# Performance work log

Measured on AMD Instinct MI355X. Metric: run time of the kernel, lower is better.

## Reference

```python
import jax, jax.numpy as jnp
import numpy as np
from jax import lax

B, T, C = 8, 1025, 512
HEADS = 8
CACHE = 256          # int(dim * cache_ratio)
CLS = 1
L = 256              # gr_cache memory length
H = W = 32           # sqrt(T - CLS)
EPS = 1e-5


def setup_inputs() -> dict:
    key = jax.random.key(0)
    ks = jax.random.split(key, 40)
    def w(k, shape, scale=0.02):
        return jax.random.normal(k, shape, dtype=jnp.float32) * scale
    inp = {}
    inp['x'] = jax.random.normal(ks[0], (B, T, C), dtype=jnp.float32)
    inp['gr_cache'] = jax.random.normal(ks[1], (1, L, CACHE), dtype=jnp.float32)
    # self-attention (dim=512) params, weights stored (in, out)
    inp['Wq1'] = w(ks[2], (C, C)); inp['bq1'] = jnp.zeros((C,), jnp.float32)
    inp['Wk1'] = w(ks[3], (C, C)); inp['bk1'] = jnp.zeros((C,), jnp.float32)
    inp['Wv1'] = w(ks[4], (C, C)); inp['bv1'] = jnp.zeros((C,), jnp.float32)
    inp['Wo1'] = w(ks[5], (C, C)); inp['bo1'] = jnp.zeros((C,), jnp.float32)
    # memory attention (dim=cache_dim=256) params
    inp['Wq2'] = w(ks[6], (CACHE, CACHE)); inp['bq2'] = jnp.zeros((CACHE,), jnp.float32)
    inp['Wk2'] = w(ks[7], (CACHE, CACHE)); inp['bk2'] = jnp.zeros((CACHE,), jnp.float32)
    inp['Wv2'] = w(ks[8], (CACHE, CACHE)); inp['bv2'] = jnp.zeros((CACHE,), jnp.float32)
    inp['Wo2'] = w(ks[9], (CACHE, CACHE)); inp['bo2'] = jnp.zeros((CACHE,), jnp.float32)
    # GRU-style gate linears: in = 2*cache_dim, out = cache_dim
    inp['Wr'] = w(ks[10], (2 * CACHE, CACHE)); inp['br'] = jnp.zeros((CACHE,), jnp.float32)
    inp['Wz'] = w(ks[11], (2 * CACHE, CACHE)); inp['bz'] = jnp.zeros((CACHE,), jnp.float32)
    inp['Wa'] = w(ks[12], (2 * CACHE, CACHE)); inp['ba'] = jnp.zeros((CACHE,), jnp.float32)
    # LayerNorm(cache_dim)
    inp['gamma'] = jnp.ones((CACHE,), jnp.float32)
    inp['beta'] = jnp.zeros((CACHE,), jnp.float32)
    # per-head gate logits, init to -1 as in the module
    inp['lam'] = jnp.full((HEADS,), -1.0, dtype=jnp.float32)
    # grouped conv pos-emb: Conv2d(512, 512, k=3, groups=CACHE) -> (O=512, I/g=2, 3, 3)
    inp['conv_w'] = w(ks[13], (C, C // CACHE, 3, 3))
    inp['conv_b'] = jnp.zeros((C,), jnp.float32)
    return inp


def _mha(q_in, kv_in, Wq, bq, Wk, bk, Wv, bv, Wo, bo):
    Bq, Tq, D = q_in.shape
    Tk = kv_in.shape[1]
    dh = D // HEADS
    q = (q_in @ Wq + bq).reshape(Bq, Tq, HEADS, dh)
    k = (kv_in @ Wk + bk).reshape(Bq, Tk, HEADS, dh)
    v = (kv_in @ Wv + bv).reshape(Bq, Tk, HEADS, dh)
    s = jnp.einsum('bqhd,bkhd->bhqk', q, k) * (1.0 / np.sqrt(dh)).astype(np.float32)
    a = jax.nn.softmax(s, axis=-1)
    o = jnp.einsum('bhqk,bkhd->bqhd', a, v).reshape(Bq, Tq, D)
    return o @ Wo + bo


def reference(x, gr_cache, Wq1, bq1, Wk1, bk1, Wv1, bv1, Wo1, bo1,
              Wq2, bq2, Wk2, bk2, Wv2, bv2, Wo2, bo2,
              Wr, br, Wz, bz, Wa, ba, gamma, beta, lam, conv_w, conv_b):
    B_, T_, C_ = x.shape
    # ---- spatial positional embedding (faithful to torch view->permute quirk) ----
    tok = x[:, CLS:, :].reshape(B_, H, W, C_).transpose(0, 3, 1, 2)   # (B, C, H, W)
    pos = lax.conv_general_dilated(tok, conv_w, (1, 1), 'SAME',
                                   feature_group_count=CACHE,
                                   dimension_numbers=('NCHW', 'OIHW', 'NCHW'))
    pos = pos + conv_b[None, :, None, None]
    pos = pos.reshape(B_, C_, T_ - CLS).transpose(0, 2, 1)            # (B, T-1, C)
    pos = jnp.concatenate([jnp.zeros((B_, CLS, C_), pos.dtype), pos], axis=1)
    # ---- self attention ----
    x_self = _mha(x, x, Wq1, bq1, Wk1, bk1, Wv1, bv1, Wo1, bo1)       # (B, T, C)
    x_self_h = x_self.reshape(B_, T_, HEADS, C_ // HEADS)
    # ---- GRU-style gated cache update ----
    gr = jnp.broadcast_to(gr_cache, (B_, L, CACHE))
    x_summary = x_self[:, :, :CACHE]
    idx = (jnp.arange(L) * T_) // L                                   # nearest interpolate T -> L
    x_summary = x_summary[:, idx, :]                                  # (B, L, CACHE)
    cat = jnp.concatenate([gr, x_summary], axis=-1)
    reset = jax.nn.sigmoid(cat @ Wr + br)
    z = jax.nn.sigmoid(cat @ Wz + bz)
    cat2 = jnp.concatenate([reset * gr, x_summary], axis=-1)
    add = jax.nn.gelu(cat2 @ Wa + ba, approximate=False)
    mu = add.mean(-1, keepdims=True)
    var = ((add - mu) ** 2).mean(-1, keepdims=True)
    add = (add - mu) / jnp.sqrt(var + EPS) * gamma + beta             # LayerNorm
    gr_new = z * add + (1.0 - z) * gr
    # ---- memory attention on first cache_dim channels ----
    x_mem = _mha(x[:, :, :CACHE], gr_new, Wq2, bq2, Wk2, bk2, Wv2, bv2, Wo2, bo2)
    x_mem = x_mem.reshape(B_, T_, HEADS, CACHE // HEADS)
    # ---- per-head alpha blend with zero-padded mem branch ----
    alpha = jax.nn.sigmoid(lam).reshape(1, 1, HEADS, 1)
    pad = jnp.zeros((B_, T_, HEADS, (C_ - CACHE) // HEADS), x.dtype)
    out = (alpha * jnp.concatenate([x_mem, pad], axis=-1)
           + (1.0 - alpha) * x_self_h).reshape(B_, T_, C_) + pos
    return out
```

## Files before the change

### kernel.cpp

```cpp
#include <hip/hip_runtime.h>
#include <math.h>

typedef unsigned short u16;
typedef unsigned int u32;
typedef __attribute__((ext_vector_type(8))) short short8;
typedef __attribute__((ext_vector_type(4))) short short4v;
typedef __attribute__((ext_vector_type(4))) float f32x4;

constexpr int Bc = 8;
constexpr int Tt = 1025;
constexpr int Cc = 512;
constexpr int Hn = 8;
constexpr int CA = 256;
constexpr int Ll = 256;

#if __has_builtin(__builtin_amdgcn_exp2f)
#define EXP2F __builtin_amdgcn_exp2f
#else
#define EXP2F exp2f
#endif

__device__ __forceinline__ u16 f2bf(float f) {
  u32 u = __builtin_bit_cast(u32, f);
  u = (u + 0x7FFFu + ((u >> 16) & 1u)) >> 16;
  return (u16)u;
}
__device__ __forceinline__ u32 pack2f(float lo, float hi) {
  const u32 a = __builtin_bit_cast(u32, hi) + 0x8000u;
  const u32 b = __builtin_bit_cast(u32, lo) + 0x8000u;
  return __builtin_amdgcn_perm(a, b, 0x07060302u);
}

__device__ __forceinline__ void gld16(void* lds, const void* g) {
  __builtin_amdgcn_global_load_lds(
      (const __attribute__((address_space(1))) u32*)g,
      (__attribute__((address_space(3))) u32*)lds, 16, 0, 0);
}

__device__ __forceinline__ int xcd_work() {
  const int nwg = gridDim.x * gridDim.y;
  const int hw = blockIdx.y * gridDim.x + blockIdx.x;
  const int q = nwg >> 3, r = nwg & 7;
  const int xcd = hw & 7, pos = hw >> 3;
  const int base = (xcd < r) ? xcd * (q + 1) : r * (q + 1) + (xcd - r) * q;
  return base + pos;
}

struct WC { const float* s; u16* d; int sN; int sK; int kshift; int tot; };
struct WCP { WC w[11]; };

__global__ void wcast_k(WCP p) {
  const WC a = p.w[blockIdx.y];
  const int kmask = (1 << a.kshift) - 1;
  for (int idx = blockIdx.x * 256 + threadIdx.x; idx < a.tot; idx += gridDim.x * 256) {
    const int k = idx & kmask;
    const int n = idx >> a.kshift;
    a.d[idx] = (k < a.sK) ? f2bf(a.s[(size_t)k * a.sN + n]) : (u16)0;
  }
}

__global__ __launch_bounds__(256) void xcast_k(const float* __restrict__ x,
                                               u16* __restrict__ xb)
{
  const size_t base = ((size_t)blockIdx.x * 256 + threadIdx.x) * 8;
  if (base >= (size_t)8200 * 512) return;
  const float4 f0 = *(const float4*)(x + base);
  const float4 f1 = *(const float4*)(x + base + 4);
  short8 w;
  ((u32*)&w)[0] = pack2f(f0.x, f0.y);
  ((u32*)&w)[1] = pack2f(f0.z, f0.w);
  ((u32*)&w)[2] = pack2f(f1.x, f1.y);
  ((u32*)&w)[3] = pack2f(f1.z, f1.w);
  *(short8*)(xb + base) = w;
}

enum { EP_NONE = 0, EP_SIGMOID = 1, EP_GELU = 2 };

struct GemmEpi {
  const float* bias[4];
  int start[4];
  float scale[4];
  int nreg;
};

template <int OUTBF, int ACT, int NH>
__global__ __launch_bounds__(256) void gemm_mfma(
    const void* __restrict__ Av, int lda,
    const u16* __restrict__ Wt,
    GemmEpi epi,
    void* __restrict__ Cout,
    int M, int N, int K)
{
  __shared__ __align__(16) u16 As[2][NH][128][32];
  __shared__ __align__(16) u16 Bs[2][NH][128][32];
  const int tid = threadIdx.x;
  const int work = xcd_work();
  const int m0 = (work / gridDim.x) * 128, n0 = (work % gridDim.x) * 128;
  const int ln = tid & 15, quad = (tid >> 4) & 3, wv = tid >> 6;
  const int wm = (wv & 1) * 64, wn = (wv >> 1) * 64;
  const int lane = tid & 63;
  const int grow = wv * 32 + (lane >> 2);
  const int gcol = (lane & 3) * 8;

  f32x4 zf = {0.f, 0.f, 0.f, 0.f};
  f32x4 acc[4][4];
  #pragma unroll
  for (int i = 0; i < 4; i++)
    #pragma unroll
    for (int j = 0; j < 4; j++) acc[i][j] = zf;

  auto issueA = [&](int t, int db) {
    const int k0 = t * (NH * 32);
    #pragma unroll
    for (int h = 0; h < NH; h++)
      #pragma unroll
      for (int i = 0; i < 2; i++)
        gld16(&As[db][h][wv * 32 + i * 16][0],
              (const u16*)Av + (size_t)(m0 + grow + i * 16) * lda + k0 + h * 32 + gcol);
  };
  auto issueB = [&](int t, int db) {
    const int k0 = t * (NH * 32);
    #pragma unroll
    for (int h = 0; h < NH; h++)
      #pragma unroll
      for (int i = 0; i < 2; i++)
        gld16(&Bs[db][h][wv * 32 + i * 16][0],
              Wt + (size_t)(n0 + grow + i * 16) * K + k0 + h * 32 + gcol);
  };

  const int NT = K / (NH * 32);
  issueA(0, 0);
  issueB(0, 0);
  __syncthreads();
  for (int t = 0; t < NT; t++) {
    const int db = t & 1;
    short8 af[NH][4], bf[NH][4];
    #pragma unroll
    for (int h = 0; h < NH; h++) {
      #pragma unroll
      for (int i = 0; i < 4; i++) af[h][i] = *(const short8*)&As[db][h][wm + i * 16 + ln][quad * 8];
      #pragma unroll
      for (int j = 0; j < 4; j++) bf[h][j] = *(const short8*)&Bs[db][h][wn + j * 16 + ln][quad * 8];
    }
    __builtin_amdgcn_sched_barrier(0);
    if (t + 1 < NT) { issueA(t + 1, db ^ 1); issueB(t + 1, db ^ 1); }
    #pragma unroll
    for (int h = 0; h < NH; h++)
      #pragma unroll
      for (int i = 0; i < 4; i++)
        #pragma unroll
        for (int j = 0; j < 4; j++)
          acc[i][j] = __builtin_amdgcn_mfma_f32_16x16x32_bf16(af[h][i], bf[h][j], acc[i][j], 0, 0, 0);
    if (t + 1 < NT) __syncthreads();
  }

  int ri = 0;
  #pragma unroll
  for (int i = 1; i < 4; i++)
    if (i < epi.nreg && epi.start[i] <= n0) ri = i;
  const float* bp = epi.bias[ri] - epi.start[ri];
  const float sc = epi.scale[ri];

  float bj[4];
  #pragma unroll
  for (int j = 0; j < 4; j++) bj[j] = bp[n0 + wn + j * 16 + ln];

  #pragma unroll
  for (int i = 0; i < 4; i++) {
    #pragma unroll
    for (int r = 0; r < 4; r++) {
      const int gm = m0 + wm + i * 16 + quad * 4 + r;
      if (gm >= M) continue;
      #pragma unroll
      for (int j = 0; j < 4; j++) {
        float v = (acc[i][j][r] + bj[j]) * sc;
        if (ACT == EP_SIGMOID)   v = 1.f / (1.f + __expf(-v));
        else if (ACT == EP_GELU) v = 0.5f * v * (1.f + erff(v * 0.70710678118654752f));
        const size_t off = (size_t)gm * N + n0 + wn + j * 16 + ln;
        if (OUTBF) ((u16*)Cout)[off] = f2bf(v);
        else       ((float*)Cout)[off] = v;
      }
    }
  }
}

template <int DH>
__global__ __launch_bounds__(256) void attn_mfma(
    const u16* __restrict__ Qp, const u16* __restrict__ Kp,
    const u16* __restrict__ Vp, u16* __restrict__ Op,
    int Tq, int Tk, int qbs, int kbs, int obs, int qrs, int krs, int ors)
{
  constexpr int NC = DH / 32;
  constexpr int NM = DH / 16;
  constexpr int VTE = 2 * DH * 32;
  constexpr int PAY = 2 * NM * 4 + 2;
  constexpr int PSTR = PAY | 1;

  __shared__ __align__(16) char smem[2 * VTE * 2 + 4 * 1024 * 2];
  static_assert(128 * PSTR * 4 <= 2 * VTE * 2 + 4 * 1024 * 2, "combine fits");
  u16* const VtP = (u16*)smem;
  u16* const PbP = (u16*)(smem + 2 * VTE * 2);

  const int work = xcd_work();
  const int bh = work / gridDim.x;
  const int b = bh >> 3, h = bh & 7;
  const int q0 = (work % gridDim.x) * 64;
  const int tid = threadIdx.x;
  const int wv = tid >> 6;
  const int pair = wv >> 1;
  const int wvp = wv & 1;
  const int lane = tid & 63;
  const int ln = lane & 15, quad = lane >> 4;
  const int lt = tid & 127;

  const u16* Qb = Qp + (size_t)b * qbs + h * DH;
  const u16* Kb = Kp + (size_t)b * kbs + h * DH;
  const u16* Vb = Vp + (size_t)b * kbs + h * DH;
  u16* Ob = Op + (size_t)b * obs + h * DH;

  const short8 z8 = {0, 0, 0, 0, 0, 0, 0, 0};
  const f32x4 zf = {0.f, 0.f, 0.f, 0.f};

  short8 qf[2][NC];
  #pragma unroll
  for (int qs = 0; qs < 2; qs++) {
    const int gq = q0 + wvp * 32 + qs * 16 + ln;
    #pragma unroll
    for (int c = 0; c < NC; c++) {
      if (gq < Tq) qf[qs][c] = *(const short8*)(Qb + (size_t)gq * qrs + c * 32 + quad * 8);
      else         qf[qs][c] = z8;
    }
  }

  f32x4 oacc[2][NM];
  float lsum[2] = {0.f, 0.f};
  #pragma unroll
  for (int qs = 0; qs < 2; qs++)
    #pragma unroll
    for (int c = 0; c < NM; c++) oacc[qs][c] = zf;

  const int vd0 = (lt & 15) * (DH / 16);
  const int vk = (lt >> 4) * 4;
  const int gb = vk >> 3, off = vk & 7;

  const int nfull = Tk >> 5;
  const int nit = (Tk + 31) >> 5;
  const int tkm1 = Tk - 1;
  const int np = (nit + 1) >> 1;
  const int it0 = pair * np;
  const int itE = it0 + np;

  auto loadK = [&](int it, short8 (&kf)[2][NC]) {
    #pragma unroll
    for (int kc = 0; kc < 2; kc++)
      #pragma unroll
      for (int c = 0; c < NC; c++) {
        int row = (it << 5) + kc * 16 + ln;
        row = row < tkm1 ? row : tkm1;
        kf[kc][c] = *(const short8*)(Kb + (size_t)row * krs + c * 32 + quad * 8);
      }
  };
  auto loadV = [&](int it, short4v (&vr)[4]) {
    #pragma unroll
    for (int i2 = 0; i2 < 4; i2++) {
      int gk = (it << 5) + vk + i2;
      gk = gk < tkm1 ? gk : tkm1;
      short4v t = {0, 0, 0, 0};
      if (DH == 64) {
        t = *(const short4v*)(Vb + (size_t)gk * krs + vd0);
      } else {
        ushort2 u = *(const ushort2*)(Vb + (size_t)gk * krs + vd0);
        t[0] = (short)u.x; t[1] = (short)u.y;
      }
      vr[i2] = t;
    }
  };

  auto body = [&](int it, short8 (&kfC)[2][NC], short4v (&vrC)[4],
                  short8 (&kfN)[2][NC], short4v (&vrN)[4]) {
    const bool full = (it < nfull);
    u16* vt = VtP + pair * VTE + (it & 1) * (DH * 32);
    const int k0 = it << 5;

    #pragma unroll
    for (int i = 0; i < DH / 16; i++) {
      const int d = vd0 + i;
      const int h2 = (d ^ (d >> 3)) & 3;
      short4v w = {vrC[0][i], vrC[1][i], vrC[2][i], vrC[3][i]};
      *(short4v*)&vt[d * 32 + ((gb ^ h2) << 3) + off] = w;
    }
    if (it + 1 < itE) { loadK(it + 1, kfN); loadV(it + 1, vrN); }
    __syncthreads();

    #pragma unroll
    for (int qs = 0; qs < 2; qs++) {
      #pragma unroll
      for (int kc = 0; kc < 2; kc++) {
        f32x4 s = zf;
        #pragma unroll
        for (int c = 0; c < NC; c++)
          s = __builtin_amdgcn_mfma_f32_16x16x32_bf16(kfC[kc][c], qf[qs][c], s, 0, 0, 0);
        float p0, p1, p2, p3;
        if (full) {
          p0 = EXP2F(s[0]); p1 = EXP2F(s[1]); p2 = EXP2F(s[2]); p3 = EXP2F(s[3]);
        } else {
          const int kb = k0 + kc * 16 + quad * 4;
          p0 = (kb + 0 < Tk) ? EXP2F(s[0]) : 0.f;
          p1 = (kb + 1 < Tk) ? EXP2F(s[1]) : 0.f;
          p2 = (kb + 2 < Tk) ? EXP2F(s[2]) : 0.f;
          p3 = (kb + 3 < Tk) ? EXP2F(s[3]) : 0.f;
        }
        lsum[qs] += (p0 + p1) + (p2 + p3);
        short4v pw;
        ((u32*)&pw)[0] = pack2f(p0, p1);
        ((u32*)&pw)[1] = pack2f(p2, p3);
        const int q = qs * 16 + ln;
        const int g = ((kc * 2 + (quad >> 1)) ^ (ln & 3)) & 3;
        *(short4v*)&PbP[wv * 1024 + q * 32 + (g << 3) + (quad & 1) * 4] = pw;
      }
    }

    short8 pf2[2];
    #pragma unroll
    for (int qs = 0; qs < 2; qs++) {
      const int q = qs * 16 + ln;
      const int g = quad ^ (ln & 3);
      pf2[qs] = *(const short8*)&PbP[wv * 1024 + q * 32 + g * 8];
    }
    #pragma unroll
    for (int c = 0; c < NM; c++) {
      const int d = c * 16 + ln;
      const int g = quad ^ ((d ^ (d >> 3)) & 3);
      const short8 vf = *(const short8*)&vt[d * 32 + g * 8];
      #pragma unroll
      for (int qs = 0; qs < 2; qs++)
        oacc[qs][c] = __builtin_amdgcn_mfma_f32_16x16x32_bf16(pf2[qs], vf, oacc[qs][c], 0, 0, 0);
    }
  };

  short8 kfA[2][NC], kfB[2][NC];
  short4v vrA[4], vrB[4];
  loadK(it0, kfA);
  loadV(it0, vrA);

  int j = it0;
  for (; j + 1 < itE; j += 2) {
    body(j, kfA, vrA, kfB, vrB);
    body(j + 1, kfB, vrB, kfA, vrA);
  }
  if (j < itE) body(j, kfA, vrA, kfB, vrB);

  __syncthreads();
  float* const cbuf = (float*)smem;
  if (wv >= 2) {
    float* dst = cbuf + ((wv - 2) * 64 + lane) * PSTR;
    int idx = 0;
    #pragma unroll
    for (int qs = 0; qs < 2; qs++)
      #pragma unroll
      for (int c = 0; c < NM; c++)
        #pragma unroll
        for (int r = 0; r < 4; r++) dst[idx++] = oacc[qs][c][r];
    dst[idx++] = lsum[0];
    dst[idx]   = lsum[1];
  }
  __syncthreads();
  if (wv >= 2) return;
  {
    const float* src = cbuf + (wv * 64 + lane) * PSTR;
    int idx = 0;
    #pragma unroll
    for (int qs = 0; qs < 2; qs++)
      #pragma unroll
      for (int c = 0; c < NM; c++)
        #pragma unroll
        for (int r = 0; r < 4; r++) oacc[qs][c][r] += src[idx++];
    lsum[0] += src[idx++];
    lsum[1] += src[idx];
  }

  float lq[2];
  #pragma unroll
  for (int qs = 0; qs < 2; qs++) {
    float t = lsum[qs];
    t += __shfl_xor(t, 16);
    t += __shfl_xor(t, 32);
    lq[qs] = t;
  }
  #pragma unroll
  for (int qs = 0; qs < 2; qs++) {
    #pragma unroll
    for (int r = 0; r < 4; r++) {
      const float linv = 1.f / __shfl(lq[qs], quad * 4 + r);
      const int gq = q0 + wvp * 32 + qs * 16 + quad * 4 + r;
      if (gq >= Tq) continue;
      #pragma unroll
      for (int c = 0; c < NM; c++)
        Ob[(size_t)gq * ors + c * 16 + ln] = f2bf(oacc[qs][c][r] * linv);
    }
  }
}

__global__ __launch_bounds__(256) void conv_combine(
    const float* __restrict__ x, const float* __restrict__ cw,
    const float* __restrict__ cb, const float* __restrict__ x_self,
    const float* __restrict__ x_mem, const float* __restrict__ lam,
    float* __restrict__ out)
{
  const int bh = blockIdx.x;
  const int b = bh >> 5, hh = bh & 31;
  const int c = (blockIdx.y << 8) + threadIdx.x;
  const int ci = c & ~1;
  const int dd = c & 63;
  const int h8 = c >> 6;
  const float alpha = 1.f / (1.f + __expf(-lam[h8]));
  const float bias = cb[c];

  float wgt[2][9];
  #pragma unroll
  for (int ch = 0; ch < 2; ch++)
    #pragma unroll
    for (int k = 0; k < 9; k++) wgt[ch][k] = cw[c * 18 + ch * 9 + k];

  const float* xrow[3];
  bool rv[3];
  #pragma unroll
  for (int r = 0; r < 3; r++) {
    const int h2 = hh + r - 1;
    rv[r] = (unsigned)h2 < 32u;
    xrow[r] = x + ((size_t)(b * Tt) + 1 + h2 * 32) * Cc + ci;
  }

  float2 win[3][3];
  #pragma unroll
  for (int r = 0; r < 3; r++) {
    win[r][0] = make_float2(0.f, 0.f);
    win[r][1] = rv[r] ? *(const float2*)(xrow[r]) : make_float2(0.f, 0.f);
  }

  const size_t bT = (size_t)b * Tt;
  for (int w = 0; w < 32; w++) {
    #pragma unroll
    for (int r = 0; r < 3; r++)
      win[r][2] = (rv[r] && w + 1 < 32) ? *(const float2*)(xrow[r] + (w + 1) * Cc)
                                        : make_float2(0.f, 0.f);
    float pos = bias;
    #pragma unroll
    for (int r = 0; r < 3; r++)
      #pragma unroll
      for (int col = 0; col < 3; col++) {
        pos += win[r][col].x * wgt[0][r * 3 + col];
        pos += win[r][col].y * wgt[1][r * 3 + col];
      }
    const size_t bt = bT + 1 + hh * 32 + w;
    const float mem = (dd < 32) ? x_mem[bt * 256 + h8 * 32 + dd] : 0.f;
    out[bt * 512 + c] = pos + alpha * mem + (1.f - alpha) * x_self[bt * 512 + c];
    #pragma unroll
    for (int r = 0; r < 3; r++) { win[r][0] = win[r][1]; win[r][1] = win[r][2]; }
  }

  if (hh == 0) {
    const float mem = (dd < 32) ? x_mem[bT * 256 + h8 * 32 + dd] : 0.f;
    out[bT * 512 + c] = alpha * mem + (1.f - alpha) * x_self[bT * 512 + c];
  }
}

__global__ void build_cat(const float* __restrict__ gr_cache,
                          const float* __restrict__ x_self,
                          u16* __restrict__ cat)
{
  const int idx = blockIdx.x * 256 + threadIdx.x;
  if (idx >= Bc * Ll * 512) return;
  const int k = idx & 511;
  const int bi = idx >> 9;
  const int i = bi & 255;
  const int b = bi >> 8;
  float v;
  if (k < 256) v = gr_cache[i * 256 + k];
  else         v = x_self[((size_t)(b * Tt + 4 * i)) * Cc + (k - 256)];
  cat[idx] = f2bf(v);
}

__global__ void build_cat2(const float* __restrict__ gr_cache,
                           const float* __restrict__ rzg,
                           u16* __restrict__ cat)
{
  const int idx = blockIdx.x * 256 + threadIdx.x;
  if (idx >= Bc * Ll * 256) return;
  const int k = idx & 255;
  const int bi = idx >> 8;
  const int i = bi & 255;
  cat[(size_t)bi * 512 + k] = f2bf(gr_cache[i * 256 + k] * rzg[(size_t)bi * 512 + k]);
}

__device__ inline float block_sum256(float v, float* red)
{
  #pragma unroll
  for (int o = 32; o >= 1; o >>= 1) v += __shfl_down(v, o);
  const int wid = threadIdx.x >> 6;
  if ((threadIdx.x & 63) == 0) red[wid] = v;
  __syncthreads();
  const float t = red[0] + red[1] + red[2] + red[3];
  __syncthreads();
  return t;
}

__global__ __launch_bounds__(256) void ln_gate(
    const float* __restrict__ add_raw, const float* __restrict__ rzg,
    const float* __restrict__ gr_cache, const float* __restrict__ gamma,
    const float* __restrict__ beta, u16* __restrict__ gr_new)
{
  __shared__ float red[4];
  const int bi = blockIdx.x;
  const int i = bi & 255;
  const int c = threadIdx.x;
  const float v = add_raw[(size_t)bi * 256 + c];
  const float mu = block_sum256(v, red) * (1.f / 256.f);
  const float dv = v - mu;
  const float var = block_sum256(dv * dv, red) * (1.f / 256.f);
  const float nrm = dv * rsqrtf(var + 1e-5f) * gamma[c] + beta[c];
  const float zz = rzg[(size_t)bi * 512 + 256 + c];
  gr_new[(size_t)bi * 256 + c] = f2bf(zz * nrm + (1.f - zz) * gr_cache[i * 256 + c]);
}

extern "C" void kernel_launch(void* const* d_in, const int* in_sizes, int n_in,
                              void* d_out, int out_size, void* d_ws, size_t ws_size,
                              hipStream_t stream)
{
  const float* x        = (const float*)d_in[0];
  const float* gr_cache = (const float*)d_in[1];
  const float* Wq1 = (const float*)d_in[2];  const float* bq1 = (const float*)d_in[3];
  const float* Wk1 = (const float*)d_in[4];  const float* bk1 = (const float*)d_in[5];
  const float* Wv1 = (const float*)d_in[6];  const float* bv1 = (const float*)d_in[7];
  const float* Wo1 = (const float*)d_in[8];  const float* bo1 = (const float*)d_in[9];
  const float* Wq2 = (const float*)d_in[10]; const float* bq2 = (const float*)d_in[11];
  const float* Wk2 = (const float*)d_in[12]; const float* bk2 = (const float*)d_in[13];
  const float* Wv2 = (const float*)d_in[14]; const float* bv2 = (const float*)d_in[15];
  const float* Wo2 = (const float*)d_in[16]; const float* bo2 = (const float*)d_in[17];
  const float* Wr  = (const float*)d_in[18]; const float* br  = (const float*)d_in[19];
  const float* Wz  = (const float*)d_in[20]; const float* bz  = (const float*)d_in[21];
  const float* Wa  = (const float*)d_in[22]; const float* ba  = (const float*)d_in[23];
  const float* gamma = (const float*)d_in[24];
  const float* beta  = (const float*)d_in[25];
  const float* lam   = (const float*)d_in[26];
  const float* conv_w = (const float*)d_in[27];
  const float* conv_b = (const float*)d_in[28];
  float* out = (float*)d_out;

  const int M1 = Bc * Tt;
  const int M2 = Bc * Ll;
  const size_t BLA = (size_t)Bc * Ll * CA;
  const size_t BL2 = (size_t)Bc * Ll * 512;

  char* W = (char*)d_ws;
  u16*   qkvq  = (u16*)(W + 0);
  u16*   xb    = (u16*)(W + 29388800);
  u16*   att1  = (u16*)(W + 29388800);
  u16*   att2  = (u16*)(W + 29388800);
  float* x_self= (float*)(W + 37785600);
  u16*   cat   = (u16*)(W + 54579200);
  float* rzg   = (float*)(W + 56676352);
  float* addr_ = (float*)(W + 60870656);
  float* x_mem = (float*)(W + 54579200);
  u16*   gr_new= (u16*)(W + 62976000);
  u16*   k2v2  = (u16*)(W + 64024576);
  u16*   wtb   = (u16*)(W + 66121728);

  u16* megaW = wtb;
  u16* o1W   = wtb + 917504;
  u16* rzW   = wtb + 1179648;
  u16* aW    = wtb + 1441792;
  u16* kvW   = wtb + 1572864;
  u16* o2W   = wtb + 1703936;

  const dim3 blk(256);

  {
    WCP p;
    p.w[0]  = {Wq1, megaW + 0,           512, 512, 9, 512 * 512};
    p.w[1]  = {Wk1, megaW + 512 * 512,   512, 512, 9, 512 * 512};
    p.w[2]  = {Wv1, megaW + 1024 * 512,  512, 512, 9, 512 * 512};
    p.w[3]  = {Wq2, megaW + 1536 * 512,  256, 256, 9, 256 * 512};
    p.w[4]  = {Wo1, o1W,                 512, 512, 9, 512 * 512};
    p.w[5]  = {Wr,  rzW + 0,             256, 512, 9, 256 * 512};
    p.w[6]  = {Wz,  rzW + 256 * 512,     256, 512, 9, 256 * 512};
    p.w[7]  = {Wa,  aW,                  256, 512, 9, 256 * 512};
    p.w[8]  = {Wk2, kvW + 0,             256, 256, 8, 256 * 256};
    p.w[9]  = {Wv2, kvW + 256 * 256,     256, 256, 8, 256 * 256};
    p.w[10] = {Wo2, o2W,                 256, 256, 8, 256 * 256};
    wcast_k<<<dim3(64, 11), blk, 0, stream>>>(p);
  }

  xcast_k<<<dim3(2050), blk, 0, stream>>>(x, xb);

  const float sQ1 = 0.18033688011112042f;
  const float sQ2 = 0.25503490664918414f;

  {
    GemmEpi e;
    e.bias[0] = bq1; e.start[0] = 0;    e.scale[0] = sQ1;
    e.bias[1] = bk1; e.start[1] = 512;  e.scale[1] = 1.f;
    e.bias[2] = bv1; e.start[2] = 1024; e.scale[2] = 1.f;
    e.bias[3] = bq2; e.start[3] = 1536; e.scale[3] = sQ2;
    e.nreg = 4;
    gemm_mfma<1, EP_NONE, 1><<<dim3(14, 65), blk, 0, stream>>>(
        xb, 512, megaW, e, qkvq, M1, 1792, 512);
  }

  attn_mfma<64><<<dim3(17, 64), dim3(256), 0, stream>>>(
      qkvq, qkvq + 512, qkvq + 1024, att1, Tt, Tt,
      Tt * 1792, Tt * 1792, Tt * 512, 1792, 1792, 512);

  {
    GemmEpi e; e.bias[0] = bo1; e.start[0] = 0; e.scale[0] = 1.f; e.nreg = 1;
    gemm_mfma<0, EP_NONE, 2><<<dim3(4, 65), blk, 0, stream>>>(
        att1, 512, o1W, e, x_self, M1, 512, 512);
  }

  build_cat<<<(int)((BL2 + 255) / 256), blk, 0, stream>>>(gr_cache, x_self, cat);
  {
    GemmEpi e;
    e.bias[0] = br; e.start[0] = 0;   e.scale[0] = 1.f;
    e.bias[1] = bz; e.start[1] = 256; e.scale[1] = 1.f;
    e.nreg = 2;
    gemm_mfma<0, EP_SIGMOID, 2><<<dim3(4, 16), blk, 0, stream>>>(
        cat, 512, rzW, e, rzg, M2, 512, 512);
  }
  build_cat2<<<(int)((BLA + 255) / 256), blk, 0, stream>>>(gr_cache, rzg, cat);
  {
    GemmEpi e; e.bias[0] = ba; e.start[0] = 0; e.scale[0] = 1.f; e.nreg = 1;
    gemm_mfma<0, EP_GELU, 2><<<dim3(2, 16), blk, 0, stream>>>(
        cat, 512, aW, e, addr_, M2, 256, 512);
  }
  ln_gate<<<M2, blk, 0, stream>>>(addr_, rzg, gr_cache, gamma, beta, gr_new);

  {
    GemmEpi e;
    e.bias[0] = bk2; e.start[0] = 0;   e.scale[0] = 1.f;
    e.bias[1] = bv2; e.start[1] = 256; e.scale[1] = 1.f;
    e.nreg = 2;
    gemm_mfma<1, EP_NONE, 2><<<dim3(4, 16), blk, 0, stream>>>(
        gr_new, 256, kvW, e, k2v2, M2, 512, 256);
  }

  attn_mfma<32><<<dim3(17, 64), dim3(256), 0, stream>>>(
      qkvq + 1536, k2v2, k2v2 + 256, att2, Tt, Ll,
      Tt * 1792, Ll * 512, Tt * 256, 1792, 512, 256);

  {
    GemmEpi e; e.bias[0] = bo2; e.start[0] = 0; e.scale[0] = 1.f; e.nreg = 1;
    gemm_mfma<0, EP_NONE, 2><<<dim3(2, 65), blk, 0, stream>>>(
        att2, 256, o2W, e, x_mem, M1, 256, 256);
  }

  conv_combine<<<dim3(Bc * 32, 2), blk, 0, stream>>>(x, conv_w, conv_b, x_self,
                                                     x_mem, lam, out);
}
```

Measured before the change: 331.0 us.

## Split self-attention key range across two blocks with atomic fp32 accumulation

The self-attention kernel now gets a grid z-dimension of 2, so each block covers half of the key range, with the two wave pairs splitting that half again. Unnormalized partial outputs and row sums are atomically added into zeroed fp32 buffers, and a separate normalize kernel divides and casts the result to bf16. The goal is more blocks to fill the GPU, at the cost of an extra zeroing kernel, heavy global atomic traffic, and an extra pass over an fp32 buffer. The kernel appears to add partial sums without a max rescale, which only works if the original already used a fixed offset instead of an online max.

Measured after the change: 355.0 us. +7.3%, slower.

```diff
diff --git a/kernel.cpp b/kernel.cpp
--- a/kernel.cpp
+++ b/kernel.cpp
@@ -74,6 +74,37 @@
   *(short8*)(xb + base) = w;
 }
 
+__global__ __launch_bounds__(256) void zero2_k(float4* a, int na4, float4* b, int nb4)
+{
+  const int i = blockIdx.x * 256 + threadIdx.x;
+  const float4 z = make_float4(0.f, 0.f, 0.f, 0.f);
+  if (i < na4) a[i] = z;
+  const int j = i - na4;
+  if (j >= 0 && j < nb4) b[j] = z;
+}
+
+__global__ __launch_bounds__(256) void attnorm_k(const float* __restrict__ xacc,
+                                                 const float* __restrict__ lacc,
+                                                 u16* __restrict__ att1)
+{
+  const size_t base = ((size_t)blockIdx.x * 256 + threadIdx.x) * 8;
+  if (base >= (size_t)8200 * 512) return;
+  const int row = (int)(base >> 9);
+  const int col = (int)(base & 511);
+  const int b = row / 1025;
+  const int q = row - b * 1025;
+  const int h = col >> 6;
+  const float linv = 1.f / lacc[(b * 8 + h) * 1025 + q];
+  const float4 f0 = *(const float4*)(xacc + base);
+  const float4 f1 = *(const float4*)(xacc + base + 4);
+  u16 w[8];
+  w[0] = f2bf(f0.x * linv); w[1] = f2bf(f0.y * linv);
+  w[2] = f2bf(f0.z * linv); w[3] = f2bf(f0.w * linv);
+  w[4] = f2bf(f1.x * linv); w[5] = f2bf(f1.y * linv);
+  w[6] = f2bf(f1.z * linv); w[7] = f2bf(f1.w * linv);
+  *(short8*)(att1 + base) = *(short8*)w;
+}
+
 enum { EP_NONE = 0, EP_SIGMOID = 1, EP_GELU = 2 };
 
 struct GemmEpi {
@@ -184,10 +215,11 @@
   }
 }
 
-template <int DH>
+template <int DH, int SPLIT>
 __global__ __launch_bounds__(256) void attn_mfma(
     const u16* __restrict__ Qp, const u16* __restrict__ Kp,
     const u16* __restrict__ Vp, u16* __restrict__ Op,
+    float* __restrict__ Xa, float* __restrict__ La,
     int Tq, int Tk, int qbs, int kbs, int obs, int qrs, int krs, int ors)
 {
   constexpr int NC = DH / 32;
@@ -205,6 +237,7 @@
   const int bh = work / gridDim.x;
   const int b = bh >> 3, h = bh & 7;
   const int q0 = (work % gridDim.x) * 64;
+  const int z = SPLIT ? blockIdx.z : 0;
   const int tid = threadIdx.x;
   const int wv = tid >> 6;
   const int pair = wv >> 1;
@@ -246,8 +279,10 @@
   const int nfull = Tk >> 5;
   const int nit = (Tk + 31) >> 5;
   const int tkm1 = Tk - 1;
-  const int np = (nit + 1) >> 1;
-  const int it0 = pair * np;
+  const int nseg = SPLIT ? 4 : 2;
+  const int np = (nit + nseg - 1) / nseg;
+  const int seg = SPLIT ? (z * 2 + pair) : pair;
+  const int it0 = seg * np;
   const int itE = it0 + np;
 
   auto loadK = [&](int it, short8 (&kf)[2][NC]) {
@@ -387,16 +422,35 @@
     t += __shfl_xor(t, 32);
     lq[qs] = t;
   }
-  #pragma unroll
-  for (int qs = 0; qs < 2; qs++) {
-    #pragma unroll
-    for (int r = 0; r < 4; r++) {
-      const float linv = 1.f / __shfl(lq[qs], quad * 4 + r);
-      const int gq = q0 + wvp * 32 + qs * 16 + quad * 4 + r;
-      if (gq >= Tq) continue;
-      #pragma unroll
-      for (int c = 0; c < NM; c++)
-        Ob[(size_t)gq * ors + c * 16 + ln] = f2bf(oacc[qs][c][r] * linv);
+
+  if (SPLIT) {
+    float* xa = Xa + (size_t)b * Tq * ors + h * DH;
+    float* la = La + (size_t)bh * Tq;
+    #pragma unroll
+    for (int qs = 0; qs < 2; qs++) {
+      #pragma unroll
+      for (int r = 0; r < 4; r++) {
+        const float lrow = __shfl(lq[qs], quad * 4 + r);
+        const int gq = q0 + wvp * 32 + qs * 16 + quad * 4 + r;
+        if (gq >= Tq) continue;
+        if (ln == 0) atomicAdd(la + gq, lrow);
+        #pragma unroll
+        for (int c = 0; c < NM; c++)
+          atomicAdd(xa + (size_t)gq * ors + c * 16 + ln, oacc[qs][c][r]);
+      }
+    }
+  } else {
+    #pragma unroll
+    for (int qs = 0; qs < 2; qs++) {
+      #pragma unroll
+      for (int r = 0; r < 4; r++) {
+        const float linv = 1.f / __shfl(lq[qs], quad * 4 + r);
+        const int gq = q0 + wvp * 32 + qs * 16 + quad * 4 + r;
+        if (gq >= Tq) continue;
+        #pragma unroll
+        for (int c = 0; c < NM; c++)
+          Ob[(size_t)gq * ors + c * 16 + ln] = f2bf(oacc[qs][c][r] * linv);
+      }
     }
   }
 }
@@ -557,11 +611,13 @@
   u16*   xb    = (u16*)(W + 29388800);
   u16*   att1  = (u16*)(W + 29388800);
   u16*   att2  = (u16*)(W + 29388800);
+  float* xacc  = (float*)(W + 37785600);
   float* x_self= (float*)(W + 37785600);
   u16*   cat   = (u16*)(W + 54579200);
   float* rzg   = (float*)(W + 56676352);
   float* addr_ = (float*)(W + 60870656);
   float* x_mem = (float*)(W + 54579200);
+  float* lacc  = (float*)(W + 62976000);
   u16*   gr_new= (u16*)(W + 62976000);
   u16*   k2v2  = (u16*)(W + 64024576);
   u16*   wtb   = (u16*)(W + 66121728);
@@ -592,6 +648,8 @@
   }
 
   xcast_k<<<dim3(2050), blk, 0, stream>>>(x, xb);
+  zero2_k<<<dim3(4165), blk, 0, stream>>>((float4*)xacc, 8200 * 512 / 4,
+                                          (float4*)lacc, 64 * 1025 / 4);
 
   const float sQ1 = 0.18033688011112042f;
   const float sQ2 = 0.25503490664918414f;
@@ -607,9 +665,10 @@
         xb, 512, megaW, e, qkvq, M1, 1792, 512);
   }
 
-  attn_mfma<64><<<dim3(17, 64), dim3(256), 0, stream>>>(
-      qkvq, qkvq + 512, qkvq + 1024, att1, Tt, Tt,
+  attn_mfma<64, 1><<<dim3(17, 64, 2), dim3(256), 0, stream>>>(
+      qkvq, qkvq + 512, qkvq + 1024, att1, xacc, lacc, Tt, Tt,
       Tt * 1792, Tt * 1792, Tt * 512, 1792, 1792, 512);
+  attnorm_k<<<dim3(2050), blk, 0, stream>>>(xacc, lacc, att1);
 
   {
     GemmEpi e; e.bias[0] = bo1; e.start[0] = 0; e.scale[0] = 1.f; e.nreg = 1;
@@ -643,8 +702,8 @@
         gr_new, 256, kvW, e, k2v2, M2, 512, 256);
   }
 
-  attn_mfma<32><<<dim3(17, 64), dim3(256), 0, stream>>>(
-      qkvq + 1536, k2v2, k2v2 + 256, att2, Tt, Ll,
+  attn_mfma<32, 0><<<dim3(17, 64), dim3(256), 0, stream>>>(
+      qkvq + 1536, k2v2, k2v2 + 256, att2, nullptr, nullptr, Tt, Ll,
       Tt * 1792, Ll * 512, Tt * 256, 1792, 512, 256);
 
   {
```
